# Kernel optimization log

Hardware: AMD Instinct MI355X
Metric: run time of the kernel (lower is better)

## Reference

```python
import jax, jax.numpy as jnp
import numpy as np

T, B = 512, 256
OBS, ACT, HID, HF = 128, 32, 512, 512
IN = OBS + ACT  # GRUCell input: stoch_dim + action_dim
LOG2PI = float(np.log(2.0 * np.pi))


def _lin(key, out_f, in_f):
    k1, k2 = jax.random.split(key)
    s = 1.0 / np.sqrt(in_f)
    w = jax.random.uniform(k1, (out_f, in_f), jnp.float32, -s, s)
    b = jax.random.uniform(k2, (out_f,), jnp.float32, -s, s)
    return w, b


def setup_inputs() -> dict:
    key = jax.random.key(0)
    ks = jax.random.split(key, 16)
    obs = jax.random.normal(ks[0], (T, B, OBS), jnp.float32)
    action = jax.random.normal(ks[1], (T, B, ACT), jnp.float32)
    reward = jax.random.normal(ks[2], (T, B, 1), jnp.float32)
    w_ih, b_ih = _lin(ks[3], 3 * HID, IN)
    w_hh, b_hh = _lin(ks[4], 3 * HID, HID)
    ow0, ob0 = _lin(ks[5], HF, HID); ow1, ob1 = _lin(ks[6], HF, HF); ow2, ob2 = _lin(ks[7], OBS, HF)
    aw0, ab0 = _lin(ks[8], HF, HID); aw1, ab1 = _lin(ks[9], HF, HF); aw2, ab2 = _lin(ks[10], ACT, HF)
    rw0, rb0 = _lin(ks[11], HF, HID); rw1, rb1 = _lin(ks[12], HF, HF); rw2, rb2 = _lin(ks[13], 1, HF)
    return dict(obs=obs, action=action, reward=reward,
                w_ih=w_ih, w_hh=w_hh, b_ih=b_ih, b_hh=b_hh,
                ow0=ow0, ob0=ob0, ow1=ow1, ob1=ob1, ow2=ow2, ob2=ob2,
                aw0=aw0, ab0=ab0, aw1=aw1, ab1=ab1, aw2=aw2, ab2=ab2,
                rw0=rw0, rb0=rb0, rw1=rw1, rb1=rb1, rw2=rw2, rb2=rb2)


def _gru(x, h, w_ih, w_hh, b_ih, b_hh):
    # PyTorch GRUCell math
    gi = x @ w_ih.T + b_ih
    gh = h @ w_hh.T + b_hh
    ir, iz, inn = jnp.split(gi, 3, axis=-1)
    hr, hz, hn = jnp.split(gh, 3, axis=-1)
    r = jax.nn.sigmoid(ir + hr)
    z = jax.nn.sigmoid(iz + hz)
    n = jnp.tanh(inn + r * hn)
    return (1.0 - z) * n + z * h


def _mlp(x, w0, b0, w1, b1, w2, b2):
    x = jax.nn.elu(x @ w0.T + b0)
    x = jax.nn.elu(x @ w1.T + b1)
    return x @ w2.T + b2


def _logprob(x, mu):
    # Normal(mu, 1).log_prob(x)
    return -0.5 * (x - mu) ** 2 - 0.5 * LOG2PI


def reference(obs, action, reward,
              w_ih, w_hh, b_ih, b_hh,
              ow0, ob0, ow1, ob1, ow2, ob2,
              aw0, ab0, aw1, ab1, aw2, ab2,
              rw0, rb0, rw1, rb1, rw2, rb2):
    # initial h: GRUCell(cat([obs[0], zeros]), h=0)
    x0 = jnp.concatenate([obs[0], jnp.zeros_like(action[0])], axis=-1)
    h0 = _gru(x0, jnp.zeros((B, HID), obs.dtype), w_ih, w_hh, b_ih, b_hh)
    xseq = jnp.concatenate([obs, action], axis=-1)  # [T, B, IN]

    def step(h, x):
        return _gru(x, h, w_ih, w_hh, b_ih, b_hh), h  # emit h BEFORE update

    _, hs = jax.lax.scan(step, h0, xseq)  # hs[i] = hidden used at step i, [T, B, HID]

    pre_obs = _mlp(hs, ow0, ob0, ow1, ob1, ow2, ob2)  # [T, B, OBS]
    obs_loss = -jnp.sum(_logprob(obs, pre_obs)) / (T * B)

    pre_action = _mlp(jax.lax.stop_gradient(hs), aw0, ab0, aw1, ab1, aw2, ab2)  # [T, B, ACT]
    action_loss = -jnp.sum(_logprob(action, pre_action)) / (T * B)

    pre_reward = _mlp(hs, rw0, rb0, rw1, rb1, rw2, rb2)  # [T, B, 1]
    # NOTE: faithful to original bug: reward_dis.log_prob(_action), broadcasting [T,B,1] vs [T,B,ACT]
    reward_loss = -jnp.sum(_logprob(action, pre_reward)) / (T * B)

    loss = obs_loss + action_loss + reward_loss
    return loss, pre_obs, pre_action, pre_reward
```

## Files before the change

kernel.cpp:

```cpp
#include <hip/hip_runtime.h>
#include <math.h>

#define TT 512
#define BB 256
#define OBS 128
#define ACT 32
#define HID 512
#define AUX_SC 0x11

typedef unsigned short u16;
typedef unsigned int u32;
typedef __attribute__((ext_vector_type(8))) short bf16x8;
typedef __attribute__((ext_vector_type(4))) float f32x4;

__device__ __forceinline__ u16 f2bf(float v) {
  u32 u = __float_as_uint(v);
  u = (u + 0x7fff + ((u >> 16) & 1)) >> 16;
  return (u16)u;
}

__device__ __forceinline__ float fast_sigmoid(float x) {
  return 1.f / (1.f + __expf(-x));
}
__device__ __forceinline__ float fast_tanh(float x) {
  float e = __expf(-2.f * fabsf(x));
  float t = (1.f - e) / (1.f + e);
  return copysignf(t, x);
}


__global__ void k_init(double* acc, int* bars, u32* zb) {
  int tid = threadIdx.x;
  if (tid == 0) acc[0] = 0.0;
  if (tid < 16) bars[tid * 64] = 0;
  zb[tid] = 0;
}

__global__ void k_convert_pad(const float* __restrict__ src, u16* __restrict__ dst,
                              int M, int K, int Mp, int Kp) {
  const int n = Mp * Kp;
  for (int idx = blockIdx.x * blockDim.x + threadIdx.x; idx < n;
       idx += gridDim.x * blockDim.x) {
    int m = idx / Kp, k = idx - m * Kp;
    float v = (m < M && k < K) ? src[(size_t)m * K + k] : 0.f;
    dst[idx] = f2bf(v);
  }
}

__global__ void k_prep_w(const float* __restrict__ w_ih, const float* __restrict__ w_hh,
                         const float* __restrict__ b_ih, const float* __restrict__ b_hh,
                         u16* __restrict__ Wr, u16* __restrict__ Wz,
                         u16* __restrict__ Wnh, u16* __restrict__ Wni,
                         float* __restrict__ bias4) {
  const int stride = gridDim.x * blockDim.x;
  const int t0 = blockIdx.x * blockDim.x + threadIdx.x;
  for (int idx = t0; idx < 512 * 704; idx += stride) {
    int j = idx / 704, k = idx - j * 704;
    float vr, vz;
    if (k < 512)      { vr = w_hh[(size_t)j * 512 + k];        vz = w_hh[(size_t)(512 + j) * 512 + k]; }
    else if (k < 672) { vr = w_ih[(size_t)j * 160 + (k - 512)]; vz = w_ih[(size_t)(512 + j) * 160 + (k - 512)]; }
    else              { vr = 0.f; vz = 0.f; }
    Wr[idx] = f2bf(vr); Wz[idx] = f2bf(vz);
  }
  for (int idx = t0; idx < 512 * 512; idx += stride) {
    int j = idx >> 9, k = idx & 511;
    Wnh[idx] = f2bf(w_hh[(size_t)(1024 + j) * 512 + k]);
  }
  for (int idx = t0; idx < 512 * 192; idx += stride) {
    int j = idx / 192, k = idx - j * 192;
    Wni[idx] = f2bf(k < 160 ? w_ih[(size_t)(1024 + j) * 160 + k] : 0.f);
  }
  for (int idx = t0; idx < 2048; idx += stride) {
    int g = idx >> 9, j = idx & 511;
    float v = (g == 0) ? b_ih[j] + b_hh[j]
            : (g == 1) ? b_ih[512 + j] + b_hh[512 + j]
            : (g == 2) ? b_ih[1024 + j] : b_hh[1024 + j];
    bias4[idx] = v;
  }
}

__global__ void k_pack_x(const float* __restrict__ obs, const float* __restrict__ action,
                         u16* __restrict__ Xb) {
  const int n = TT * BB * 160;
  for (int idx = blockIdx.x * blockDim.x + threadIdx.x; idx < n;
       idx += gridDim.x * blockDim.x) {
    int rr = idx / 160, cc = idx - rr * 160;
    int t = rr / BB, b = rr - t * BB;
    float v;
    if (t == 0) v = (cc < OBS) ? obs[(size_t)b * OBS + cc] : 0.f;
    else        v = (cc < OBS) ? obs[((size_t)(t - 1) * BB + b) * OBS + cc]
                               : action[((size_t)(t - 1) * BB + b) * ACT + (cc - OBS)];
    Xb[idx] = f2bf(v);
  }
}

__global__ __launch_bounds__(256, 1) void k_gru_seq(
    const u16* __restrict__ Wr, const u16* __restrict__ Wz,
    const u16* __restrict__ Wnh, const u16* __restrict__ Wni,
    const float* __restrict__ bias4, const u16* __restrict__ Xb,
    u16* __restrict__ hs,
    float* __restrict__ h32c,
    const u16* __restrict__ zb,
    int* __restrict__ bars,
    int t0, int TC)
{
  __shared__ u16 Bs[67584];
  __shared__ __align__(16) char scratch[22528];
  u16* As = (u16*)scratch;
  float* red = (float*)scratch;

  const int jt = blockIdx.x, bt = blockIdx.y;
  const int tid = threadIdx.x, w = tid >> 6, lane = tid & 63;
  const int m16 = lane & 15, q = lane >> 4;

  for (int i = w; i < 132; i += 4) {
    int fc = i * 64 + lane;
    const u16* g;
    if (fc < 5632) {
      int loc = (fc < 2816) ? fc : fc - 2816;
      int jj = loc / 88, c = loc - jj * 88;
      int cg = c ^ (jj & 7);
      const u16* W = (fc < 2816) ? Wr : Wz;
      g = W + ((size_t)(jt * 32 + jj) * 704 + cg * 8);
    } else if (fc < 7680) {
      int loc = fc - 5632;
      int jj = loc >> 6, c = loc & 63;
      int cg = c ^ (jj & 7);
      g = Wnh + ((size_t)(jt * 32 + jj) * 512 + cg * 8);
    } else {
      int loc = fc - 7680;
      int jj = loc / 24, c = loc - jj * 24;
      int cg = c ^ (jj & 7);
      g = Wni + ((size_t)(jt * 32 + jj) * 192 + cg * 8);
    }
    __builtin_amdgcn_global_load_lds((const __attribute__((address_space(1))) u32*)g,
        (__attribute__((address_space(3))) u32*)(Bs + i * 512), 16, 0, 0);
  }

  int aFlag[6]; u32 aOff[6];
  const int nAI = (w < 2) ? 6 : 5;
  for (int n2 = 0; n2 < 6; ++n2) { aFlag[n2] = 2; aOff[n2] = 0; }
  for (int n2 = 0; n2 < nAI; ++n2) {
    int fc = (w + 4 * n2) * 64 + lane;
    int r = fc / 88, c = fc - r * 88;
    int cg = c ^ (r & 7);
    int b = bt * 16 + r;
    if (cg < 64)      { aFlag[n2] = 0; aOff[n2] = (u32)b * 512 + cg * 8; }
    else if (cg < 84) { aFlag[n2] = 1; aOff[n2] = (u32)b * 160 + (cg - 64) * 8; }
  }

  const int eb = tid >> 4;
  const int j0 = (tid & 15) * 2;
  const int gj = jt * 32 + j0;
  const int gb = bt * 16 + eb;
  const float br0 = bias4[gj],        br1 = bias4[gj + 1];
  const float bz0 = bias4[512 + gj],  bz1 = bias4[512 + gj + 1];
  const float bi0 = bias4[1024 + gj], bi1 = bias4[1024 + gj + 1];
  const float bh0 = bias4[1536 + gj], bh1 = bias4[1536 + gj + 1];
  float hv0 = 0.f, hv1 = 0.f;
  if (t0 > 0) { hv0 = h32c[(size_t)gb * 512 + gj]; hv1 = h32c[(size_t)gb * 512 + gj + 1]; }

  const int ti = j0 >> 4, c0 = j0 & 15;

  for (int s = 0; s < TC; ++s) {
    const int t = t0 + s;
    const int sp = (s == 0) ? TC - 1 : s - 1;
    const u16* hsrc = hs + (size_t)sp * BB * 512;
    const u16* xsrc = Xb + (size_t)t * BB * 160;
    const bool hzero = (t == 0);

    for (int n2 = 0; n2 < nAI; ++n2) {
      const u16* g = (aFlag[n2] == 0) ? (hzero ? zb : hsrc + aOff[n2])
                   : (aFlag[n2] == 1) ? (xsrc + aOff[n2]) : zb;
      __builtin_amdgcn_global_load_lds((const __attribute__((address_space(1))) u32*)g,
          (__attribute__((address_space(3))) u32*)(As + (w + 4 * n2) * 512), 16, 0, AUX_SC);
    }
    __syncthreads();

    f32x4 acc[8];
#pragma unroll
    for (int ct = 0; ct < 8; ++ct) acc[ct] = (f32x4){0.f, 0.f, 0.f, 0.f};
    for (int ks = w; ks < 21; ks += 4) {
      int cb = ks * 4 + q;
      bf16x8 af = *(const bf16x8*)&As[(size_t)m16 * 704 + (cb ^ (m16 & 7)) * 8];
#pragma unroll
      for (int h2 = 0; h2 < 2; ++h2) {
        int jj = h2 * 16 + m16;
        int sw = (cb ^ (jj & 7)) * 8;
        bf16x8 b0 = *(const bf16x8*)&Bs[(size_t)jj * 704 + sw];
        acc[h2] = __builtin_amdgcn_mfma_f32_16x16x32_bf16(af, b0, acc[h2], 0, 0, 0);
        bf16x8 b1 = *(const bf16x8*)&Bs[22528 + (size_t)jj * 704 + sw];
        acc[2 + h2] = __builtin_amdgcn_mfma_f32_16x16x32_bf16(af, b1, acc[2 + h2], 0, 0, 0);
      }
      if (ks < 16) {
#pragma unroll
        for (int h2 = 0; h2 < 2; ++h2) {
          int jj = h2 * 16 + m16;
          bf16x8 b2 = *(const bf16x8*)&Bs[45056 + (size_t)jj * 512 + (cb ^ (jj & 7)) * 8];
          acc[4 + h2] = __builtin_amdgcn_mfma_f32_16x16x32_bf16(af, b2, acc[4 + h2], 0, 0, 0);
        }
      } else {
        int cb2 = (ks - 16) * 4 + q;
#pragma unroll
        for (int h2 = 0; h2 < 2; ++h2) {
          int jj = h2 * 16 + m16;
          bf16x8 b3 = *(const bf16x8*)&Bs[61440 + (size_t)jj * 192 + (cb2 ^ (jj & 7)) * 8];
          acc[6 + h2] = __builtin_amdgcn_mfma_f32_16x16x32_bf16(af, b3, acc[6 + h2], 0, 0, 0);
        }
      }
    }
    __syncthreads();

    {
      float* myred = red + (w & 1) * 2048;
      if (w < 2) {
#pragma unroll
        for (int ct = 0; ct < 8; ++ct)
#pragma unroll
          for (int p = 0; p < 4; ++p) myred[ct * 256 + (q * 4 + p) * 16 + m16] = acc[ct][p];
      }
      __syncthreads();
      if (w >= 2) {
#pragma unroll
        for (int ct = 0; ct < 8; ++ct)
#pragma unroll
          for (int p = 0; p < 4; ++p) {
            int o = ct * 256 + (q * 4 + p) * 16 + m16;
            myred[o] += acc[ct][p];
          }
      }
      __syncthreads();
    }

    {
#define RD(ctt, cc) (red[(ctt)*256 + eb*16 + (cc)] + red[2048 + (ctt)*256 + eb*16 + (cc)])
      float rs0 = RD(ti, c0),     rs1 = RD(ti, c0 + 1);
      float zs0 = RD(2 + ti, c0), zs1 = RD(2 + ti, c0 + 1);
      float nh0 = RD(4 + ti, c0), nh1 = RD(4 + ti, c0 + 1);
      float ni0 = RD(6 + ti, c0), ni1 = RD(6 + ti, c0 + 1);
#undef RD
      float r0 = fast_sigmoid(rs0 + br0);
      float z0 = fast_sigmoid(zs0 + bz0);
      float n0 = fast_tanh(ni0 + bi0 + r0 * (nh0 + bh0));
      float h0 = (1.f - z0) * n0 + z0 * hv0;
      float r1 = fast_sigmoid(rs1 + br1);
      float z1 = fast_sigmoid(zs1 + bz1);
      float n1 = fast_tanh(ni1 + bi1 + r1 * (nh1 + bh1));
      float h1 = (1.f - z1) * n1 + z1 * hv1;
      hv0 = h0; hv1 = h1;
      u32 pk = (u32)f2bf(h0) | ((u32)f2bf(h1) << 16);
      __hip_atomic_store((u32*)&hs[((size_t)s * BB + gb) * 512 + gj], pk,
                         __ATOMIC_RELAXED, __HIP_MEMORY_SCOPE_AGENT);
    }

    __syncthreads();
    if (tid == 0) {
      __hip_atomic_fetch_add(&bars[bt * 64], 1, __ATOMIC_RELAXED, __HIP_MEMORY_SCOPE_AGENT);
      const int target = 16 * (t + 1);
      while (__hip_atomic_load(&bars[bt * 64], __ATOMIC_RELAXED, __HIP_MEMORY_SCOPE_AGENT) < target)
        __builtin_amdgcn_s_sleep(1);
    }
    __syncthreads();
  }

  h32c[(size_t)gb * 512 + gj] = hv0;
  h32c[(size_t)gb * 512 + gj + 1] = hv1;
}

__global__ __launch_bounds__(256) void k_mfma_gemm(
    const u16* __restrict__ A, const u16* __restrict__ B,
    const float* __restrict__ bias,
    float* __restrict__ outf, u16* __restrict__ outb,
    int N, int K, int M, int act)
{
  __shared__ u16 As[128 * 64];
  __shared__ u16 Bs[128 * 64];
  const int bn = blockIdx.y * 128;
  const int bm = blockIdx.x * 128;
  const int tid = threadIdx.x;
  const int w = tid >> 6, lane = tid & 63;
  const int wr = w >> 1, wc = w & 1;

  f32x4 acc[4][4];
#pragma unroll
  for (int i = 0; i < 4; ++i)
#pragma unroll
    for (int j = 0; j < 4; ++j) acc[i][j] = (f32x4){0.f, 0.f, 0.f, 0.f};

  const int lr8 = lane >> 3;
  const int lc8 = lane & 7;

  for (int kt = 0; kt < K; kt += 64) {
    __syncthreads();
#pragma unroll
    for (int i = 0; i < 4; ++i) {
      int r0 = (w * 4 + i) * 8;
      int r = r0 + lr8;
      int c = lc8 ^ (r & 7);
      const u16* ga = A + (size_t)(bn + r) * K + kt + c * 8;
      const u16* gb = B + (size_t)(bm + r) * K + kt + c * 8;
      __builtin_amdgcn_global_load_lds((const __attribute__((address_space(1))) u32*)ga,
                                       (__attribute__((address_space(3))) u32*)(As + r0 * 64), 16, 0, 0);
      __builtin_amdgcn_global_load_lds((const __attribute__((address_space(1))) u32*)gb,
                                       (__attribute__((address_space(3))) u32*)(Bs + r0 * 64), 16, 0, 0);
    }
    __syncthreads();

    const int m16 = lane & 15, q = lane >> 4;
#pragma unroll
    for (int kk = 0; kk < 2; ++kk) {
      bf16x8 af[4], bfr[4];
#pragma unroll
      for (int i = 0; i < 4; ++i) {
        int ra = wr * 64 + i * 16 + m16;
        af[i] = *(const bf16x8*)&As[ra * 64 + ((kk * 4 + q) ^ (ra & 7)) * 8];
        int rb = wc * 64 + i * 16 + m16;
        bfr[i] = *(const bf16x8*)&Bs[rb * 64 + ((kk * 4 + q) ^ (rb & 7)) * 8];
      }
#pragma unroll
      for (int i = 0; i < 4; ++i)
#pragma unroll
        for (int j = 0; j < 4; ++j)
          acc[i][j] = __builtin_amdgcn_mfma_f32_16x16x32_bf16(af[i], bfr[j], acc[i][j], 0, 0, 0);
    }
  }

  const int m16 = lane & 15, q = lane >> 4;
#pragma unroll
  for (int i = 0; i < 4; ++i) {
#pragma unroll
    for (int j = 0; j < 4; ++j) {
      int col = bm + wc * 64 + j * 16 + m16;
      if (col >= M) continue;
      float bs = bias[col];
#pragma unroll
      for (int p = 0; p < 4; ++p) {
        int row = bn + wr * 64 + i * 16 + q * 4 + p;
        float v = acc[i][j][p] + bs;
        if (act) v = (v > 0.f) ? v : (__expf(v) - 1.f);
        if (outf) outf[(size_t)row * M + col] = v;
        else      outb[(size_t)row * M + col] = f2bf(v);
      }
    }
  }
}

__global__ __launch_bounds__(256) void k_loss(
    const float* __restrict__ obs, const float* __restrict__ action,
    const float* __restrict__ p_obs, const float* __restrict__ p_act,
    const float* __restrict__ p_rew, double* __restrict__ acc)
{
  const long long n1 = (long long)TT * BB * OBS;
  const long long n2 = (long long)TT * BB * ACT;
  const long long n  = n1 + n2 + n2;
  const float C = 0.91893853320467274178f;
  double s = 0.0;
  for (long long idx = (long long)blockIdx.x * blockDim.x + threadIdx.x; idx < n;
       idx += (long long)gridDim.x * blockDim.x) {
    float d;
    if (idx < n1) {
      d = obs[idx] - p_obs[idx];
    } else if (idx < n1 + n2) {
      long long i = idx - n1;
      d = action[i] - p_act[i];
    } else {
      long long i = idx - n1 - n2;
      d = action[i] - p_rew[i >> 5];
    }
    s += (double)(0.5f * d * d + C);
  }
  __shared__ double red[256];
  red[threadIdx.x] = s;
  __syncthreads();
  for (int off = 128; off > 0; off >>= 1) {
    if ((int)threadIdx.x < off) red[threadIdx.x] += red[threadIdx.x + off];
    __syncthreads();
  }
  if (threadIdx.x == 0) atomicAdd(acc, red[0]);
}

__global__ void k_finalize(const double* __restrict__ acc, float* __restrict__ out) {
  if (threadIdx.x == 0) out[0] = (float)(acc[0] / (double)(TT * BB));
}


extern "C" void kernel_launch(void* const* d_in, const int* in_sizes, int n_in,
                              void* d_out, int out_size, void* d_ws, size_t ws_size,
                              hipStream_t stream) {
  const float* obs    = (const float*)d_in[0];
  const float* action = (const float*)d_in[1];
  const float* w_ih = (const float*)d_in[3];
  const float* w_hh = (const float*)d_in[4];
  const float* b_ih = (const float*)d_in[5];
  const float* b_hh = (const float*)d_in[6];
  const float* hw[9] = {(const float*)d_in[7],  (const float*)d_in[9],  (const float*)d_in[11],
                        (const float*)d_in[13], (const float*)d_in[15], (const float*)d_in[17],
                        (const float*)d_in[19], (const float*)d_in[21], (const float*)d_in[23]};
  const float* hb[9] = {(const float*)d_in[8],  (const float*)d_in[10], (const float*)d_in[12],
                        (const float*)d_in[14], (const float*)d_in[16], (const float*)d_in[18],
                        (const float*)d_in[20], (const float*)d_in[22], (const float*)d_in[24]};
  const int hM[9]  = {512, 512, 128, 512, 512, 32, 512, 512, 1};
  const int hMp[9] = {512, 512, 128, 512, 512, 128, 512, 512, 128};

  float* out     = (float*)d_out;
  float* pre_obs = out + 1;
  float* pre_act = pre_obs + (size_t)TT * BB * OBS;
  float* pre_rew = pre_act + (size_t)TT * BB * ACT;

  char* ws = (char*)d_ws;
  size_t off = 0;
  auto alloc = [&](size_t bytes) { void* p = ws + off; off = (off + bytes + 255) & ~(size_t)255; return p; };
  double* acc  = (double*)alloc(256);
  int* bars    = (int*)alloc(16 * 256);
  u32* zerobuf = (u32*)alloc(1024);
  u16* Wr  = (u16*)alloc((size_t)512 * 704 * 2);
  u16* Wz  = (u16*)alloc((size_t)512 * 704 * 2);
  u16* Wnh = (u16*)alloc((size_t)512 * 512 * 2);
  u16* Wni = (u16*)alloc((size_t)512 * 192 * 2);
  float* bias4 = (float*)alloc(2048 * 4);
  u16* headb[9];
  for (int i = 0; i < 9; ++i) headb[i] = (u16*)alloc((size_t)hMp[i] * 512 * 2);
  float* h32c = (float*)alloc((size_t)BB * 512 * 4);
  u16* Xb     = (u16*)alloc((size_t)TT * BB * 160 * 2);
  const size_t fixed = off;

  int TC = 512;
  while (TC > 8 && fixed + 3ull * TC * BB * 512 * 2ull + (1u << 20) > ws_size) TC >>= 1;
  u16* hs_chunk = (u16*)alloc((size_t)TC * BB * 512 * 2);
  u16* tmp1b    = (u16*)alloc((size_t)TC * BB * 512 * 2);
  u16* tmp2b    = (u16*)alloc((size_t)TC * BB * 512 * 2);
  const int CH = TC * BB;
  const int NCH = TT / TC;

  k_init<<<1, 256, 0, stream>>>(acc, bars, zerobuf);
  k_prep_w<<<512, 256, 0, stream>>>(w_ih, w_hh, b_ih, b_hh, Wr, Wz, Wnh, Wni, bias4);
  for (int i = 0; i < 9; ++i)
    k_convert_pad<<<512, 256, 0, stream>>>(hw[i], headb[i], hM[i], 512, hMp[i], 512);
  k_pack_x<<<4096, 256, 0, stream>>>(obs, action, Xb);

  for (int c = 0; c < NCH; ++c) {
    k_gru_seq<<<dim3(16, 16), 256, 0, stream>>>(
        Wr, Wz, Wnh, Wni, bias4, Xb, hs_chunk, h32c, (const u16*)zerobuf, bars, c * TC, TC);
    for (int h = 0; h < 3; ++h) {
      int M2 = hM[h * 3 + 2], Mp2 = hMp[h * 3 + 2];
      float* outp = (h == 0) ? pre_obs + (size_t)c * CH * OBS
                  : (h == 1) ? pre_act + (size_t)c * CH * ACT
                             : pre_rew + (size_t)c * CH;
      k_mfma_gemm<<<dim3(4, CH / 128), 256, 0, stream>>>(
          hs_chunk, headb[h * 3 + 0], hb[h * 3 + 0], nullptr, tmp1b, CH, 512, 512, 1);
      k_mfma_gemm<<<dim3(4, CH / 128), 256, 0, stream>>>(
          tmp1b, headb[h * 3 + 1], hb[h * 3 + 1], nullptr, tmp2b, CH, 512, 512, 1);
      k_mfma_gemm<<<dim3(Mp2 / 128, CH / 128), 256, 0, stream>>>(
          tmp2b, headb[h * 3 + 2], hb[h * 3 + 2], outp, nullptr, CH, 512, M2, 0);
    }
  }

  k_loss<<<2048, 256, 0, stream>>>(obs, action, pre_obs, pre_act, pre_rew, acc);
  k_finalize<<<1, 64, 0, stream>>>(acc, out);
}
```

Measured before the change: 3.609 ms.

## Split GRU recurrence across 512 blocks with per-gate warp specialization

Doubles the GRU grid from 256 to 512 persistent blocks, each owning 16 hidden units instead of 32. This halves the per-block weight tile in shared memory so two blocks can fit per CU. Three warps each handle one hidden-path gate (r, z, n_h) over K=512, and the fourth warp computes the input-path projections directly from global Xb. This replaces the split-K reduction across warps with a simple exchange buffer. The cost is twice as many blocks joining each per-step global barrier and uncached global reads of the input operand in the fourth warp.

Measured after the change: 3.275 ms. 9.2% less time.

```diff
diff --git a/kernel.cpp b/kernel.cpp
--- a/kernel.cpp
+++ b/kernel.cpp
@@ -94,7 +94,7 @@
   }
 }
 
-__global__ __launch_bounds__(256, 1) void k_gru_seq(
+__global__ __launch_bounds__(256, 2) void k_gru_seq(
     const u16* __restrict__ Wr, const u16* __restrict__ Wz,
     const u16* __restrict__ Wnh, const u16* __restrict__ Wni,
     const float* __restrict__ bias4, const u16* __restrict__ Xb,
@@ -104,63 +104,52 @@
     int* __restrict__ bars,
     int t0, int TC)
 {
-  __shared__ u16 Bs[67584];
-  __shared__ __align__(16) char scratch[22528];
-  u16* As = (u16*)scratch;
-  float* red = (float*)scratch;
-
+  __shared__ __align__(16) u16 SB[40448];
   const int jt = blockIdx.x, bt = blockIdx.y;
   const int tid = threadIdx.x, w = tid >> 6, lane = tid & 63;
   const int m16 = lane & 15, q = lane >> 4;
 
-  for (int i = w; i < 132; i += 4) {
-    int fc = i * 64 + lane;
+  for (int i = w; i < 63; i += 4) {
     const u16* g;
-    if (fc < 5632) {
-      int loc = (fc < 2816) ? fc : fc - 2816;
-      int jj = loc / 88, c = loc - jj * 88;
-      int cg = c ^ (jj & 7);
-      const u16* W = (fc < 2816) ? Wr : Wz;
-      g = W + ((size_t)(jt * 32 + jj) * 704 + cg * 8);
-    } else if (fc < 7680) {
-      int loc = fc - 5632;
-      int jj = loc >> 6, c = loc & 63;
-      int cg = c ^ (jj & 7);
-      g = Wnh + ((size_t)(jt * 32 + jj) * 512 + cg * 8);
+    if (i < 48) {
+      int gi = i >> 4, jj = i & 15;
+      int c = lane ^ (jj & 7);
+      int gjr = jt * 16 + jj;
+      g = (gi == 0) ? Wr  + (size_t)gjr * 704 + c * 8
+        : (gi == 1) ? Wz  + (size_t)gjr * 704 + c * 8
+                    : Wnh + (size_t)gjr * 512 + c * 8;
     } else {
-      int loc = fc - 7680;
-      int jj = loc / 24, c = loc - jj * 24;
-      int cg = c ^ (jj & 7);
-      g = Wni + ((size_t)(jt * 32 + jj) * 192 + cg * 8);
+      int e = (i - 48) * 64 + lane;
+      int gi = e / 320, rem = e - gi * 320;
+      int jj = rem / 20, p = rem - jj * 20;
+      int c = p - jj; if (c < 0) c += 20;
+      int gjr = jt * 16 + jj;
+      g = (gi == 0) ? Wni + (size_t)gjr * 192 + c * 8
+        : (gi == 1) ? Wr  + (size_t)gjr * 704 + 512 + c * 8
+                    : Wz  + (size_t)gjr * 704 + 512 + c * 8;
     }
     __builtin_amdgcn_global_load_lds((const __attribute__((address_space(1))) u32*)g,
-        (__attribute__((address_space(3))) u32*)(Bs + i * 512), 16, 0, 0);
-  }
-
-  int aFlag[6]; u32 aOff[6];
-  const int nAI = (w < 2) ? 6 : 5;
-  for (int n2 = 0; n2 < 6; ++n2) { aFlag[n2] = 2; aOff[n2] = 0; }
-  for (int n2 = 0; n2 < nAI; ++n2) {
-    int fc = (w + 4 * n2) * 64 + lane;
-    int r = fc / 88, c = fc - r * 88;
-    int cg = c ^ (r & 7);
-    int b = bt * 16 + r;
-    if (cg < 64)      { aFlag[n2] = 0; aOff[n2] = (u32)b * 512 + cg * 8; }
-    else if (cg < 84) { aFlag[n2] = 1; aOff[n2] = (u32)b * 160 + (cg - 64) * 8; }
+        (__attribute__((address_space(3))) u32*)(SB + i * 512), 16, 0, 0);
+  }
+
+  u32 aoff[4];
+#pragma unroll
+  for (int n = 0; n < 4; ++n) {
+    int i = w * 4 + n;
+    aoff[n] = (u32)(bt * 16 + i) * 512 + (u32)(lane ^ (i & 7)) * 8;
   }
 
   const int eb = tid >> 4;
-  const int j0 = (tid & 15) * 2;
-  const int gj = jt * 32 + j0;
-  const int gb = bt * 16 + eb;
-  const float br0 = bias4[gj],        br1 = bias4[gj + 1];
-  const float bz0 = bias4[512 + gj],  bz1 = bias4[512 + gj + 1];
-  const float bi0 = bias4[1024 + gj], bi1 = bias4[1024 + gj + 1];
-  const float bh0 = bias4[1536 + gj], bh1 = bias4[1536 + gj + 1];
-  float hv0 = 0.f, hv1 = 0.f;
-  if (t0 > 0) { hv0 = h32c[(size_t)gb * 512 + gj]; hv1 = h32c[(size_t)gb * 512 + gj + 1]; }
-
-  const int ti = j0 >> 4, c0 = j0 & 15;
+  const int ej = tid & 15;
+  const int gj = jt * 16 + ej;
+  const int gbrow = bt * 16 + eb;
+  const float br = bias4[gj], bz = bias4[512 + gj];
+  const float bi = bias4[1024 + gj], bh = bias4[1536 + gj];
+  float hv = 0.f;
+  if (t0 > 0) hv = h32c[(size_t)gbrow * 512 + gj];
+
+  u16* As = SB + 32256;
+  float* exch = (float*)(SB + 32256);
 
   for (int s = 0; s < TC; ++s) {
     const int t = t0 + s;
@@ -169,102 +158,87 @@
     const u16* xsrc = Xb + (size_t)t * BB * 160;
     const bool hzero = (t == 0);
 
-    for (int n2 = 0; n2 < nAI; ++n2) {
-      const u16* g = (aFlag[n2] == 0) ? (hzero ? zb : hsrc + aOff[n2])
-                   : (aFlag[n2] == 1) ? (xsrc + aOff[n2]) : zb;
+#pragma unroll
+    for (int n = 0; n < 4; ++n) {
+      const u16* g = hzero ? zb : hsrc + aoff[n];
       __builtin_amdgcn_global_load_lds((const __attribute__((address_space(1))) u32*)g,
-          (__attribute__((address_space(3))) u32*)(As + (w + 4 * n2) * 512), 16, 0, AUX_SC);
-    }
-    __syncthreads();
-
-    f32x4 acc[8];
-#pragma unroll
-    for (int ct = 0; ct < 8; ++ct) acc[ct] = (f32x4){0.f, 0.f, 0.f, 0.f};
-    for (int ks = w; ks < 21; ks += 4) {
-      int cb = ks * 4 + q;
-      bf16x8 af = *(const bf16x8*)&As[(size_t)m16 * 704 + (cb ^ (m16 & 7)) * 8];
-#pragma unroll
-      for (int h2 = 0; h2 < 2; ++h2) {
-        int jj = h2 * 16 + m16;
-        int sw = (cb ^ (jj & 7)) * 8;
-        bf16x8 b0 = *(const bf16x8*)&Bs[(size_t)jj * 704 + sw];
-        acc[h2] = __builtin_amdgcn_mfma_f32_16x16x32_bf16(af, b0, acc[h2], 0, 0, 0);
-        bf16x8 b1 = *(const bf16x8*)&Bs[22528 + (size_t)jj * 704 + sw];
-        acc[2 + h2] = __builtin_amdgcn_mfma_f32_16x16x32_bf16(af, b1, acc[2 + h2], 0, 0, 0);
-      }
-      if (ks < 16) {
-#pragma unroll
-        for (int h2 = 0; h2 < 2; ++h2) {
-          int jj = h2 * 16 + m16;
-          bf16x8 b2 = *(const bf16x8*)&Bs[45056 + (size_t)jj * 512 + (cb ^ (jj & 7)) * 8];
-          acc[4 + h2] = __builtin_amdgcn_mfma_f32_16x16x32_bf16(af, b2, acc[4 + h2], 0, 0, 0);
-        }
-      } else {
-        int cb2 = (ks - 16) * 4 + q;
-#pragma unroll
-        for (int h2 = 0; h2 < 2; ++h2) {
-          int jj = h2 * 16 + m16;
-          bf16x8 b3 = *(const bf16x8*)&Bs[61440 + (size_t)jj * 192 + (cb2 ^ (jj & 7)) * 8];
-          acc[6 + h2] = __builtin_amdgcn_mfma_f32_16x16x32_bf16(af, b3, acc[6 + h2], 0, 0, 0);
-        }
+          (__attribute__((address_space(3))) u32*)(As + (w * 4 + n) * 512), 16, 0, AUX_SC);
+    }
+    __syncthreads();
+
+    f32x4 acc0 = (f32x4){0.f, 0.f, 0.f, 0.f};
+    f32x4 acc1 = (f32x4){0.f, 0.f, 0.f, 0.f};
+    f32x4 acc2 = (f32x4){0.f, 0.f, 0.f, 0.f};
+    if (w < 3) {
+      const int bbase = w * 8192;
+#pragma unroll
+      for (int ks = 0; ks < 16; ++ks) {
+        int cb = ks * 4 + q;
+        int sw = (cb ^ (m16 & 7)) * 8;
+        bf16x8 af = *(const bf16x8*)&As[m16 * 512 + sw];
+        bf16x8 bf = *(const bf16x8*)&SB[bbase + m16 * 512 + sw];
+        acc0 = __builtin_amdgcn_mfma_f32_16x16x32_bf16(af, bf, acc0, 0, 0, 0);
+      }
+    } else {
+#pragma unroll
+      for (int ks = 0; ks < 5; ++ks) {
+        int cb = ks * 4 + q;
+        int pos = cb + m16; if (pos >= 20) pos -= 20;
+        bf16x8 af = *(const bf16x8*)&xsrc[m16 * 160 + cb * 8];
+        bf16x8 b0 = *(const bf16x8*)&SB[24576 + m16 * 160 + pos * 8];
+        bf16x8 b1 = *(const bf16x8*)&SB[27136 + m16 * 160 + pos * 8];
+        bf16x8 b2 = *(const bf16x8*)&SB[29696 + m16 * 160 + pos * 8];
+        acc0 = __builtin_amdgcn_mfma_f32_16x16x32_bf16(af, b0, acc0, 0, 0, 0);
+        acc1 = __builtin_amdgcn_mfma_f32_16x16x32_bf16(af, b1, acc1, 0, 0, 0);
+        acc2 = __builtin_amdgcn_mfma_f32_16x16x32_bf16(af, b2, acc2, 0, 0, 0);
+      }
+    }
+    __syncthreads();
+
+    if (w < 3) {
+#pragma unroll
+      for (int p = 0; p < 4; ++p)
+        exch[w * 256 + (q * 4 + p) * 16 + m16] = acc0[p];
+    } else {
+#pragma unroll
+      for (int p = 0; p < 4; ++p) {
+        int o = (q * 4 + p) * 16 + m16;
+        exch[768 + o]  = acc0[p];
+        exch[1024 + o] = acc1[p];
+        exch[1280 + o] = acc2[p];
       }
     }
     __syncthreads();
 
     {
-      float* myred = red + (w & 1) * 2048;
-      if (w < 2) {
-#pragma unroll
-        for (int ct = 0; ct < 8; ++ct)
-#pragma unroll
-          for (int p = 0; p < 4; ++p) myred[ct * 256 + (q * 4 + p) * 16 + m16] = acc[ct][p];
-      }
-      __syncthreads();
-      if (w >= 2) {
-#pragma unroll
-        for (int ct = 0; ct < 8; ++ct)
-#pragma unroll
-          for (int p = 0; p < 4; ++p) {
-            int o = ct * 256 + (q * 4 + p) * 16 + m16;
-            myred[o] += acc[ct][p];
-          }
-      }
-      __syncthreads();
-    }
-
-    {
-#define RD(ctt, cc) (red[(ctt)*256 + eb*16 + (cc)] + red[2048 + (ctt)*256 + eb*16 + (cc)])
-      float rs0 = RD(ti, c0),     rs1 = RD(ti, c0 + 1);
-      float zs0 = RD(2 + ti, c0), zs1 = RD(2 + ti, c0 + 1);
-      float nh0 = RD(4 + ti, c0), nh1 = RD(4 + ti, c0 + 1);
-      float ni0 = RD(6 + ti, c0), ni1 = RD(6 + ti, c0 + 1);
-#undef RD
-      float r0 = fast_sigmoid(rs0 + br0);
-      float z0 = fast_sigmoid(zs0 + bz0);
-      float n0 = fast_tanh(ni0 + bi0 + r0 * (nh0 + bh0));
-      float h0 = (1.f - z0) * n0 + z0 * hv0;
-      float r1 = fast_sigmoid(rs1 + br1);
-      float z1 = fast_sigmoid(zs1 + bz1);
-      float n1 = fast_tanh(ni1 + bi1 + r1 * (nh1 + bh1));
-      float h1 = (1.f - z1) * n1 + z1 * hv1;
-      hv0 = h0; hv1 = h1;
-      u32 pk = (u32)f2bf(h0) | ((u32)f2bf(h1) << 16);
-      __hip_atomic_store((u32*)&hs[((size_t)s * BB + gb) * 512 + gj], pk,
-                         __ATOMIC_RELAXED, __HIP_MEMORY_SCOPE_AGENT);
+      float rs  = exch[tid]        + exch[1024 + tid];
+      float zs  = exch[256 + tid]  + exch[1280 + tid];
+      float nhv = exch[512 + tid];
+      float niv = exch[768 + tid];
+      float r = fast_sigmoid(rs + br);
+      float z = fast_sigmoid(zs + bz);
+      float n = fast_tanh(niv + bi + r * (nhv + bh));
+      float h = (1.f - z) * n + z * hv;
+      hv = h;
+      float ho = __shfl_xor(h, 1);
+      if ((ej & 1) == 0) {
+        u32 pk = (u32)f2bf(h) | ((u32)f2bf(ho) << 16);
+        __hip_atomic_store((u32*)&hs[((size_t)s * BB + gbrow) * 512 + gj], pk,
+                           __ATOMIC_RELAXED, __HIP_MEMORY_SCOPE_AGENT);
+      }
     }
 
     __syncthreads();
     if (tid == 0) {
       __hip_atomic_fetch_add(&bars[bt * 64], 1, __ATOMIC_RELAXED, __HIP_MEMORY_SCOPE_AGENT);
-      const int target = 16 * (t + 1);
+      const int target = 32 * (t + 1);
       while (__hip_atomic_load(&bars[bt * 64], __ATOMIC_RELAXED, __HIP_MEMORY_SCOPE_AGENT) < target)
         __builtin_amdgcn_s_sleep(1);
     }
     __syncthreads();
   }
 
-  h32c[(size_t)gb * 512 + gj] = hv0;
-  h32c[(size_t)gb * 512 + gj + 1] = hv1;
+  h32c[(size_t)gbrow * 512 + gj] = hv;
 }
 
 __global__ __launch_bounds__(256) void k_mfma_gemm(
@@ -439,7 +413,7 @@
   k_pack_x<<<4096, 256, 0, stream>>>(obs, action, Xb);
 
   for (int c = 0; c < NCH; ++c) {
-    k_gru_seq<<<dim3(16, 16), 256, 0, stream>>>(
+    k_gru_seq<<<dim3(32, 16), 256, 0, stream>>>(
         Wr, Wz, Wnh, Wni, bias4, Xb, hs_chunk, h32c, (const u16*)zerobuf, bars, c * TC, TC);
     for (int h = 0; h < 3; ++h) {
       int M2 = hM[h * 3 + 2], Mp2 = hMp[h * 3 + 2];
```
